# Kernel tuning notes

Measured on AMD Instinct MI355X. Metric: run time of the kernel, lower is better.

Reference implementation:

```python
import jax, jax.numpy as jnp
import numpy as np

HID = 128          # hidden_dim
NEV = 16           # n_eigenvectors
CURV = 1.0         # curvature
MAX_NORM = 0.95
N_SCALES = 3


def setup_inputs() -> dict:
    key = jax.random.key(0)
    ks = jax.random.split(key, 12)
    B, N, D = 2048, 128, 64
    A = jax.random.uniform(ks[0], (B, N, N), dtype=jnp.float32)
    A = 0.5 * (A + jnp.swapaxes(A, -1, -2))  # symmetric nonnegative adjacency
    nf = jax.random.normal(ks[1], (B, N, D), dtype=jnp.float32)
    s = 0.05
    return {
        'adjacency': A,
        'node_features': nf,
        'scale_weights': jnp.ones((N_SCALES,), jnp.float32) / N_SCALES,
        'curvature_scale': jnp.array(1.0, jnp.float32),
        'sp_w1': jax.random.normal(ks[2], (NEV, HID), jnp.float32) * s,
        'sp_b1': jnp.zeros((HID,), jnp.float32),
        'sp_w2': jax.random.normal(ks[3], (HID, HID // 2), jnp.float32) * s,
        'sp_b2': jnp.zeros((HID // 2,), jnp.float32),
        'out_w1': jax.random.normal(ks[4], (HID, HID), jnp.float32) * s,
        'out_b1': jnp.zeros((HID,), jnp.float32),
        'out_w2': jax.random.normal(ks[5], (HID, 16), jnp.float32) * s,
        'out_b2': jnp.zeros((16,), jnp.float32),
    }


def reference(adjacency, node_features, scale_weights, curvature_scale,
              sp_w1, sp_b1, sp_w2, sp_b2, out_w1, out_b1, out_w2, out_b2):
    B, N, _ = adjacency.shape
    deg = adjacency.sum(axis=-1)                         # (B, N)
    # normalized Laplacian  L = I - D^{-1/2} A D^{-1/2}
    d_is = (deg + 1e-8) ** -0.5
    sym_adj = adjacency * d_is[:, :, None] * d_is[:, None, :]
    L = jnp.eye(N, dtype=adjacency.dtype) - sym_adj
    evals, evecs = jnp.linalg.eigh(L)                    # ascending, like torch
    k = min(NEV, N - 1)
    sel_vals = evals[:, 1:k + 1]                         # (B, k)  skip trivial eig
    sel_vecs = evecs[:, :, 1:k + 1]                      # (B, N, k)
    # spectral pooling: softmax over -eigenvalues, weighted sum of eigenvectors over nodes
    w = jax.nn.softmax(-sel_vals, axis=-1)               # (B, k)
    pooled = (sel_vecs * w[:, None, :]).sum(axis=1)      # (B, k)
    spectral = jnp.maximum(pooled @ sp_w1 + sp_b1, 0.0) @ sp_w2 + sp_b2  # (B, HID//2)
    # multi-scale diffusion with row-normalized adjacency
    row_adj = adjacency / (deg + 1e-8)[:, :, None]
    ws = jax.nn.softmax(scale_weights)
    feats = node_features
    ms = ws[0] * feats.mean(axis=1)                      # (B, D) with D == HID//2
    for s in range(1, N_SCALES):
        feats = jnp.einsum('bij,bjd->bid', row_adj, feats)
        ms = ms + ws[s] * feats.mean(axis=1)
    combined = jnp.concatenate([spectral, ms], axis=-1)  # (B, HID)
    z_euclidean = jnp.maximum(combined @ out_w1 + out_b1, 0.0) @ out_w2 + out_b2
    # Poincare ball projection (curvature value used as detached scalar, like .item())
    c = CURV * jax.nn.sigmoid(curvature_scale)
    c_const = jax.lax.stop_gradient(c)
    norm = jnp.linalg.norm(z_euclidean, axis=-1, keepdims=True)
    max_r = MAX_NORM / jnp.sqrt(c_const)
    z = z_euclidean * jnp.minimum(1.0, max_r / (norm + 1e-12))
    return z, z_euclidean, spectral, sel_vals, c
```

## Files before the change

### kernel.cpp

```cpp
#include <hip/hip_runtime.h>
#include <math.h>

#define NN 128
#define BLK 256

__device__ __forceinline__ float hsum4(float4 v) { return (v.x + v.y) + (v.z + v.w); }

__device__ __forceinline__ float bcast(float v, int lane) {
  return __int_as_float(__builtin_amdgcn_readlane(__float_as_int(v), lane));
}

__device__ __forceinline__ float waveRedF(float v) {
#pragma unroll
  for (int off = 32; off > 0; off >>= 1) v += __shfl_down(v, off, 64);
  return v;
}
__device__ __forceinline__ float waveAllRedF(float v) {
#pragma unroll
  for (int off = 32; off > 0; off >>= 1) v += __shfl_xor(v, off, 64);
  return v;
}
__device__ __forceinline__ float getc(float4 a, int c) {
  return (c == 0) ? a.x : (c == 1) ? a.y : (c == 2) ? a.z : a.w;
}
__device__ __forceinline__ float blockReduceSumF(float v, float* redf, int tid) {
  v = waveRedF(v);
  __syncthreads();
  if ((tid & 63) == 0) redf[tid >> 6] = v;
  __syncthreads();
  return (redf[0] + redf[1]) + (redf[2] + redf[3]);
}
__device__ __forceinline__ float startvec(int i, int k) {
  unsigned h = (unsigned)(i * 1664525 + k * 1013904223 + 12345);
  h ^= h >> 13; h *= 2654435761u; h ^= h >> 16;
  return ((float)(h & 0xFFFFFFu) * (1.0f / 16777216.0f)) - 0.5f;
}

extern "C" __global__ void __launch_bounds__(BLK, 4)
holo_kernel(const float* __restrict__ A, const float* __restrict__ F,
            const float* __restrict__ swg, const float* __restrict__ curv,
            const float* __restrict__ W1, const float* __restrict__ Bb1,
            const float* __restrict__ W2, const float* __restrict__ Bb2,
            const float* __restrict__ OW1, const float* __restrict__ OB1,
            const float* __restrict__ OW2, const float* __restrict__ OB2,
            float* __restrict__ out, int B)
{
  __shared__ __align__(16) float wsA[NN * 17];
  __shared__ __align__(16) float wsB[NN * 17];
  __shared__ unsigned swb[16 * 5];
  __shared__ float  ddf[NN], eef[NN];
  __shared__ float  tvecf[NN];
  __shared__ float  redf[4];
  __shared__ double sc[8];
  __shared__ float  redupf[2], redutf[2], redsigf[2];
  __shared__ float  lamf[20], blof[17], bhif[17];
  __shared__ float  ssvf[16], dredf[16];
  __shared__ float  msv[64], pool[16], zrow[16];

  double* dscr  = (double*)wsA;
  float* svec   = wsA + 512;
  float* invdeg = wsA + 640;
  float* gvv    = wsA + 768;
  float* cw     = wsA + 896;
  float* ubuf   = wsA + 1024;
  float* pbuf   = wsA + 1152;
  float* colk   = wsA + 1280;
  float* byv    = wsA;
  float* fscr   = wsB;
  float* cornr  = wsB + 256;
  float* sA     = wsB;
  float* comb   = wsB;
  float* hbuf   = wsB + 128;
  unsigned char* bcnt = (unsigned char*)swb;

  const int  tid  = threadIdx.x;
  const int  r    = tid & 127;
  const int  h    = tid >> 7;
  const int  lane = tid & 63;
  const int  widm = tid >> 6;
  const long b    = blockIdx.x;
  const float* Ab = A + b * (long)(NN * NN);
  const float* Fb = F + b * (long)(NN * 64);

  float4 areg[16];
  {
    const float4* Arow = reinterpret_cast<const float4*>(Ab + (long)r * NN) + 16 * h;
#pragma unroll
    for (int uu = 0; uu < 16; ++uu) areg[uu] = Arow[uu];
  }
  if (tid == 0) {
    const float a0 = swg[0], a1 = swg[1], a2 = swg[2];
    const float mx = fmaxf(a0, fmaxf(a1, a2));
    const float e0 = expf(a0 - mx), e1 = expf(a1 - mx), e2v = expf(a2 - mx);
    const float s = e0 + e1 + e2v;
    sc[0] = (double)(e0 / s); sc[1] = (double)(e1 / s); sc[2] = (double)(e2v / s);
  }
  {
    float4 s4 = make_float4(0.f, 0.f, 0.f, 0.f);
#pragma unroll
    for (int uu = 0; uu < 16; ++uu) {
      s4.x += areg[uu].x; s4.y += areg[uu].y; s4.z += areg[uu].z; s4.w += areg[uu].w;
    }
    dscr[tid] = (double)hsum4(s4);
  }
  __syncthreads();
  if (tid < NN) {
    const double dg = dscr[tid] + dscr[tid + NN] + 1e-8;
    invdeg[tid] = (float)(1.0 / dg);
    svec[tid]   = (float)(1.0 / sqrt(dg));
  }
  __syncthreads();
  {
    const float4* iv4 = (const float4*)invdeg;
    float4 acc = make_float4(0.f, 0.f, 0.f, 0.f);
#pragma unroll
    for (int uu = 0; uu < 16; ++uu) {
      const float4 a = areg[uu], w = iv4[16 * h + uu];
      acc.x = fmaf(a.x, w.x, acc.x); acc.y = fmaf(a.y, w.y, acc.y);
      acc.z = fmaf(a.z, w.z, acc.z); acc.w = fmaf(a.w, w.w, acc.w);
    }
    fscr[tid] = hsum4(acc);
  }
  __syncthreads();
  if (tid < NN) {
    const float gv = fscr[tid] + fscr[tid + NN];
    gvv[tid] = gv;
    ubuf[tid] = gv * invdeg[tid];
  }
  __syncthreads();
  {
    const float4* ub4 = (const float4*)ubuf;
    float4 acc = make_float4(0.f, 0.f, 0.f, 0.f);
#pragma unroll
    for (int uu = 0; uu < 16; ++uu) {
      const float4 a = areg[uu], w = ub4[16 * h + uu];
      acc.x = fmaf(a.x, w.x, acc.x); acc.y = fmaf(a.y, w.y, acc.y);
      acc.z = fmaf(a.z, w.z, acc.z); acc.w = fmaf(a.w, w.w, acc.w);
    }
    fscr[tid] = hsum4(acc);
  }
  __syncthreads();
  if (tid < NN) {
    const float hv = fscr[tid] + fscr[tid + NN];
    cw[tid] = ((float)sc[0] + (float)sc[1] * gvv[tid] + (float)sc[2] * hv) * (1.0f / NN);
  }
  __syncthreads();
  {
    const int d = tid & 63, qt = tid >> 6;
    float acc = 0.0f;
    const float* fb = Fb + qt * 32 * 64;
    for (int n = 0; n < 32; ++n) acc = fmaf(cw[qt * 32 + n], fb[n * 64 + d], acc);
    fscr[tid] = acc;
  }
  __syncthreads();
  if (tid < 64) msv[tid] = (fscr[tid] + fscr[64 + tid]) + (fscr[128 + tid] + fscr[192 + tid]);

  {
    const float sr = svec[r];
    const float4* sv4p = (const float4*)svec;
#pragma unroll
    for (int uu = 0; uu < 16; ++uu) {
      const float4 sv = sv4p[16 * h + uu];
      float4 a = areg[uu];
      a.x = -a.x * sr * sv.x; a.y = -a.y * sr * sv.y;
      a.z = -a.z * sr * sv.z; a.w = -a.w * sr * sv.w;
      areg[uu] = a;
    }
    if ((r >> 6) == h) {
      const int cl = r & 63, du = cl >> 2, dc = cl & 3;
#pragma unroll
      for (int uu = 0; uu < 16; ++uu) if (uu == du) {
        float4 a = areg[uu];
        a.x += (dc == 0) ? 1.f : 0.f; a.y += (dc == 1) ? 1.f : 0.f;
        a.z += (dc == 2) ? 1.f : 0.f; a.w += (dc == 3) ? 1.f : 0.f;
        areg[uu] = a;
      }
    }
  }
  if (tid < NN) tvecf[tid] = 1.0f;
  if (h == 0) {
    const float v0 = areg[0].x;
    colk[r] = v0;
    if (r == 0) ddf[0] = v0;
    const float s = waveRedF((r >= 2) ? v0 * v0 : 0.f);
    if (lane == 0) redsigf[widm] = s;
  }
  __syncthreads();

  for (int k = 0; k < 95; ++k) {
    const float sigma  = redsigf[0] + redsigf[1];
    const float alphaf = colk[k + 1];
    float betaf, tauf, sclf;
    if (sigma <= 0.f) { betaf = alphaf; tauf = 0.f; sclf = 0.f; }
    else {
      betaf = (float)(-copysign(sqrt((double)alphaf * (double)alphaf + (double)sigma),
                                (double)alphaf));
      tauf = (betaf - alphaf) / betaf;
      sclf = 1.0f / (alphaf - betaf);
    }
    if (tid == 0) eef[k] = betaf;
    if (h == 0) ubuf[r] = (r <= k) ? 0.f : (r == k + 1) ? 1.f : colk[r] * sclf;
    __syncthreads();
    {
      float4 acc = make_float4(0.f, 0.f, 0.f, 0.f);
      if (r >= k + 1 && 64 * h + 63 >= k + 1 && tauf != 0.f) {
        const float4* ub4 = (const float4*)ubuf;
#pragma unroll
        for (int uu = 0; uu < 16; ++uu) {
          if (64 * h + 4 * uu + 3 >= k + 1) {
            const float4 a = areg[uu], u4 = ub4[16 * h + uu];
            acc.x = fmaf(a.x, u4.x, acc.x); acc.y = fmaf(a.y, u4.y, acc.y);
            acc.z = fmaf(a.z, u4.z, acc.z); acc.w = fmaf(a.w, u4.w, acc.w);
          }
        }
      }
      fscr[tid] = hsum4(acc);
    }
    __syncthreads();
    if (h == 0) {
      const float p = tauf * (fscr[r] + fscr[r + NN]);
      pbuf[r] = p;
      const float uv = ubuf[r];
      const float s1 = waveRedF(uv * p);
      const float s2 = waveRedF(uv * tvecf[r]);
      if (lane == 0) { redupf[widm] = s1; redutf[widm] = s2; }
    }
    __syncthreads();
    {
      const float K   = 0.5f * tauf * (redupf[0] + redupf[1]);
      const float tut = tauf * (redutf[0] + redutf[1]);
      if (r >= k + 1) {
        const float ur = ubuf[r];
        const float qr = fmaf(-K, ur, pbuf[r]);
        if (64 * h + 63 >= k + 1) {
          const float4* ub4 = (const float4*)ubuf;
          const float4* pb4 = (const float4*)pbuf;
#pragma unroll
          for (int uu = 0; uu < 16; ++uu) {
            if (64 * h + 4 * uu + 3 >= k + 1) {
              const float4 u4 = ub4[16 * h + uu], p4 = pb4[16 * h + uu];
              float4 a = areg[uu];
              const float qx = fmaf(-K, u4.x, p4.x);
              const float qy = fmaf(-K, u4.y, p4.y);
              const float qz = fmaf(-K, u4.z, p4.z);
              const float qw = fmaf(-K, u4.w, p4.w);
              a.x -= ur * qx + qr * u4.x;
              a.y -= ur * qy + qr * u4.y;
              a.z -= ur * qz + qr * u4.z;
              a.w -= ur * qw + qr * u4.w;
              areg[uu] = a;
            }
          }
        }
        if (h == 0) tvecf[r] -= tut * ubuf[r];
      }
      const int hstar = (k + 1) >> 6;
      if (h == hstar) {
        float sigp = 0.0f;
        if (r >= k + 1) {
          const int cl = (k + 1) - 64 * hstar, du = cl >> 2, dc = cl & 3;
          float val = 0.f;
#pragma unroll
          for (int uu = 0; uu < 16; ++uu) if (uu == du) val = getc(areg[uu], dc);
          if (r == k + 1) ddf[k + 1] = val;
          else {
            colk[r] = val;
            if (r >= k + 3) sigp = val * val;
          }
        }
        const float s = waveRedF(sigp);
        if (lane == 0) redsigf[widm & 1] = s;
      }
    }
    __syncthreads();
  }

  if (h == 1 && r >= 96) {
    const int rl = r - 96;
#pragma unroll
    for (int uu = 8; uu < 16; ++uu) {
      const int j0 = (uu - 8) * 4;
      cornr[rl * 33 + j0 + 0] = areg[uu].x;
      cornr[rl * 33 + j0 + 1] = areg[uu].y;
      cornr[rl * 33 + j0 + 2] = areg[uu].z;
      cornr[rl * 33 + j0 + 3] = areg[uu].w;
    }
  }
  __syncthreads();

  if (tid < 64) {
    const bool own = (lane < 32);
    float arow[32];
#pragma unroll
    for (int j = 0; j < 32; ++j) arow[j] = own ? cornr[lane * 33 + j] : 0.f;
    float colval = own ? colk[96 + lane] : 0.f;
    float tv     = own ? tvecf[96 + lane] : 0.f;

    for (int k = 95; k <= 125; ++k) {
      const int kk = k - 95;
      const float sigp  = (lane >= kk + 1 && lane < 32) ? colval * colval : 0.f;
      const float sigma = waveAllRedF(sigp);
      const float alphaf = bcast(colval, kk);
      float betaf, tauf, sclf;
      if (sigma <= 0.f) { betaf = alphaf; tauf = 0.f; sclf = 0.f; }
      else {
        betaf = -copysignf(sqrtf(fmaf(alphaf, alphaf, sigma)), alphaf);
        tauf = (betaf - alphaf) / betaf;
        sclf = 1.0f / (alphaf - betaf);
      }
      if (lane == 0) eef[k] = betaf;
      const bool live = own && (lane >= kk);
      const float u_me = !live ? 0.f : (lane == kk ? 1.f : colval * sclf);
      float y = 0.f;
#pragma unroll
      for (int j = 0; j < 32; ++j) y = fmaf(arow[j], bcast(u_me, j), y);
      const float p_me = live ? tauf * y : 0.f;
      const float up = waveAllRedF(u_me * p_me);
      const float ut = waveAllRedF(u_me * tv);
      const float K   = 0.5f * tauf * up;
      const float tut = tauf * ut;
      const float q_me = fmaf(-K, u_me, p_me);
      tv -= tut * u_me;
      float ncol = 0.f;
#pragma unroll
      for (int j = 0; j < 32; ++j) {
        const float uj = bcast(u_me, j);
        const float qj = bcast(q_me, j);
        arow[j] -= u_me * qj + q_me * uj;
        if (j == kk) ncol = arow[j];
      }
      if (lane == 0) ddf[k + 1] = bcast(ncol, kk);
      colval = (lane > kk && lane < 32) ? ncol : 0.f;
    }
    const float e126 = bcast(colval, 31);
    const float d127 = bcast(arow[31], 31);
    if (lane == 0) { eef[NN - 2] = e126; ddf[NN - 1] = d127; }
    if (own) tvecf[96 + lane] = tv;
  }
  __syncthreads();

  if (tid == 0) {
    double lo = 1e30, hi = -1e30;
    for (int i = 0; i < NN; ++i) {
      const double rr = ((i > 0) ? fabs((double)eef[i - 1]) : 0.0)
                      + ((i < NN - 1) ? fabs((double)eef[i]) : 0.0);
      lo = fmin(lo, (double)ddf[i] - rr);
      hi = fmax(hi, (double)ddf[i] + rr);
    }
    sc[4] = lo - 1e-6; sc[5] = hi + 1e-6;
  }
  __syncthreads();
  if (tid < 17) { blof[tid] = (float)sc[4]; bhif[tid] = (float)sc[5]; }
  __syncthreads();
  for (int round = 0; round < 11; ++round) {
    if (tid < 119) {
      const int ke = tid / 7, j = tid % 7;
      const double lo = (double)blof[ke], hi = (double)bhif[ke];
      const double x = lo + (hi - lo) * ((double)(j + 1) * 0.125);
      int cnt = 0;
      double pm = 1.0, p = (double)ddf[0] - x;
      if (p < 0.0) cnt++;
      for (int i = 1; i < NN; ++i) {
        const double e = (double)eef[i - 1];
        const double pn = ((double)ddf[i] - x) * p - (e * e) * pm;
        pm = p; p = pn;
        if ((p < 0.0) != (pm < 0.0)) cnt++;
        const double ap = fabs(p);
        if (ap > 1e100)                   { p *= 1e-100; pm *= 1e-100; }
        else if (ap < 1e-100 && ap > 0.0) { p *= 1e100;  pm *= 1e100; }
      }
      bcnt[tid] = (unsigned char)cnt;
    }
    __syncthreads();
    if (tid < 17) {
      const float lo = blof[tid], hi = bhif[tid];
      const float w8 = (hi - lo) * 0.125f;
      float nlo = lo, nhi = hi;
      for (int jj = 0; jj < 7; ++jj) {
        const float x = lo + w8 * (float)(jj + 1);
        if ((int)bcnt[tid * 7 + jj] <= tid) nlo = x; else { nhi = x; break; }
      }
      blof[tid] = nlo; bhif[tid] = nhi;
    }
    __syncthreads();
  }
  if (tid < 17) lamf[tid] = 0.5f * (blof[tid] + bhif[tid]);
  __syncthreads();

  if (tid < 16) {
    const double lk = (double)lamf[tid + 1];
    for (int it = 0; it < 2; ++it) {
      float beta = (float)((double)ddf[0] - lk);
      float gam  = eef[0];
      float rr   = (it == 0) ? startvec(0, tid) : byv[0 * 17 + tid];
      unsigned bw = 0;
      for (int i = 1; i < NN; ++i) {
        const int j = i - 1;
        const float ai = eef[i - 1];
        const float bi = (float)((double)ddf[i] - lk);
        const float ci = (i < NN - 1) ? eef[i] : 0.0f;
        const float ri = (it == 0) ? startvec(i, tid) : byv[i * 17 + tid];
        if (fabsf(beta) >= fabsf(ai)) {
          float piv = (beta == 0.0f) ? 1e-25f : beta;
          const float mm = ai / piv;
          sA [j * 17 + tid] = piv;
          byv[j * 17 + tid] = rr;
          beta = bi - mm * gam;  gam = ci;  rr = ri - mm * rr;
        } else {
          const float mm = beta / ai;
          sA [j * 17 + tid] = mm;
          byv[j * 17 + tid] = ri;
          beta = gam - mm * bi;  gam = -mm * ci;  rr = rr - mm * ri;
          bw |= 1u << (j & 31);
        }
        if ((j & 31) == 31) { swb[tid * 5 + (j >> 5)] = bw; bw = 0; }
      }
      if (beta == 0.0f) beta = 1e-25f;
      sA [127 * 17 + tid] = beta;
      byv[127 * 17 + tid] = rr;
      swb[tid * 5 + 3] = bw;
      float y1 = 0.0f, y2 = 0.0f;
      for (int j = NN - 1; j >= 0; --j) {
        const bool sj = (swb[tid * 5 + (j >> 5)] >> (j & 31)) & 1;
        const bool sjm1 = (j > 0) ? ((swb[tid * 5 + ((j - 1) >> 5)] >> ((j - 1) & 31)) & 1) : false;
        float u0, u1, u2;
        if (sj) {
          u0 = eef[j];
          u1 = (float)((double)ddf[j + 1] - lk);
          u2 = (j < NN - 2) ? eef[j + 1] : 0.0f;
        } else {
          u0 = sA[j * 17 + tid];
          const float ej = (j < NN - 1) ? eef[j] : 0.0f;
          u1 = sjm1 ? (-sA[(j - 1) * 17 + tid] * ej) : ej;
          u2 = 0.0f;
        }
        const float yy = (byv[j * 17 + tid] - u1 * y1 - u2 * y2) / u0;
        byv[j * 17 + tid] = yy;
        y2 = y1; y1 = yy;
      }
      double nrm = 0.0;
      for (int i = 0; i < NN; ++i) { const double v = (double)byv[i * 17 + tid]; nrm += v * v; }
      const double inv = 1.0 / sqrt(nrm);
      for (int i = 0; i < NN; ++i) byv[i * 17 + tid] = (float)((double)byv[i * 17 + tid] * inv);
    }
  }
  __syncthreads();

  for (int kk = 1; kk < 16; ++kk) {
    const int j = tid >> 3, s8 = tid & 7;
    float part = 0.0f;
    if (j < kk)
      for (int i = s8 * 16; i < s8 * 16 + 16; ++i)
        part += byv[i * 17 + j] * byv[i * 17 + kk];
    for (int off = 4; off > 0; off >>= 1) part += __shfl_down(part, off, 8);
    __syncthreads();
    if (s8 == 0 && j < kk) dredf[j] = part;
    __syncthreads();
    if (tid < NN) {
      float acc = byv[tid * 17 + kk];
      for (int j2 = 0; j2 < kk; ++j2) acc -= dredf[j2] * byv[tid * 17 + j2];
      byv[tid * 17 + kk] = acc;
    }
    __syncthreads();
    float p2 = 0.0f;
    if (tid < NN) { const float v = byv[tid * 17 + kk]; p2 = v * v; }
    const float n2 = blockReduceSumF(p2, redf, tid);
    if (tid < NN) byv[tid * 17 + kk] = byv[tid * 17 + kk] / sqrtf(n2);
    __syncthreads();
  }

  if (tid < NN) {
    const int j = tid >> 3, s8 = tid & 7;
    float part = 0.0f;
    for (int i = s8 * 16; i < s8 * 16 + 16; ++i)
      part += tvecf[i] * byv[i * 17 + j];
    for (int off = 4; off > 0; off >>= 1) part += __shfl_down(part, off, 8);
    if (s8 == 0) ssvf[j] = part;
  }
  __syncthreads();
  if (tid == 0) {
    float lv[16], ev[16];
    float mx = -1e30f;
    for (int i = 0; i < 16; ++i) { lv[i] = lamf[i + 1]; mx = fmaxf(mx, -lv[i]); }
    float se = 0.0f;
    for (int i = 0; i < 16; ++i) { ev[i] = expf(-lv[i] - mx); se += ev[i]; }
    for (int i = 0; i < 16; ++i) pool[i] = (ev[i] / se) * ssvf[i];
  }
  __syncthreads();

  if (tid < NN) {
    float acc = Bb1[tid];
    for (int i = 0; i < 16; ++i) acc = fmaf(pool[i], W1[i * 128 + tid], acc);
    hbuf[tid] = fmaxf(acc, 0.0f);
  }
  __syncthreads();
  if (tid < 64) {
    float acc = Bb2[tid];
    for (int i = 0; i < 128; ++i) acc = fmaf(hbuf[i], W2[i * 64 + tid], acc);
    comb[tid] = acc;
  } else if (tid < NN) {
    comb[tid] = msv[tid - 64];
  }
  __syncthreads();
  if (tid < NN) {
    float acc = OB1[tid];
    for (int i = 0; i < 128; ++i) acc = fmaf(comb[i], OW1[i * 128 + tid], acc);
    hbuf[tid] = fmaxf(acc, 0.0f);
  }
  __syncthreads();
  if (tid < 16) {
    float acc = OB2[tid];
    for (int i = 0; i < 128; ++i) acc = fmaf(hbuf[i], OW2[i * 16 + tid], acc);
    zrow[tid] = acc;
  }
  __syncthreads();

  const long zeoff = (long)B * 16;
  const long spoff = (long)B * 32;
  const long svoff = (long)B * 32 + (long)B * 64;
  const long coff  = svoff + (long)B * 16;

  if (tid == 0) {
    const float c = 1.0f / (1.0f + expf(-curv[0]));
    float nrm = 0.0f;
    for (int i = 0; i < 16; ++i) nrm += zrow[i] * zrow[i];
    nrm = sqrtf(nrm);
    const float max_r = 0.95f / sqrtf(c);
    sc[3] = (double)fminf(1.0f, max_r / (nrm + 1e-12f));
    if (b == 0) out[coff] = c;
  }
  __syncthreads();
  if (tid < 16) {
    const float fac = (float)sc[3];
    out[b * 16 + tid]          = zrow[tid] * fac;
    out[zeoff + b * 16 + tid]  = zrow[tid];
    out[svoff + b * 16 + tid]  = lamf[tid + 1];
  }
  if (tid < 64) out[spoff + b * 64 + tid] = comb[tid];
}

extern "C" void kernel_launch(void* const* d_in, const int* in_sizes, int n_in,
                              void* d_out, int out_size, void* d_ws, size_t ws_size,
                              hipStream_t stream) {
  const float* A    = (const float*)d_in[0];
  const float* F    = (const float*)d_in[1];
  const float* swg  = (const float*)d_in[2];
  const float* curv = (const float*)d_in[3];
  const float* W1   = (const float*)d_in[4];
  const float* Bb1  = (const float*)d_in[5];
  const float* W2   = (const float*)d_in[6];
  const float* Bb2  = (const float*)d_in[7];
  const float* OW1  = (const float*)d_in[8];
  const float* OB1  = (const float*)d_in[9];
  const float* OW2  = (const float*)d_in[10];
  const float* OB2  = (const float*)d_in[11];
  float* out = (float*)d_out;
  const int B = in_sizes[0] / (128 * 128);

  holo_kernel<<<dim3(B), dim3(BLK), 0, stream>>>(
      A, F, swg, curv, W1, Bb1, W2, Bb2, OW1, OB1, OW2, OB2, out, B);
}
```

Measured before the change: 1.405 ms.

## Shift tridiagonalization wave-handoff earlier and fuse Gram-Schmidt norm into projection

The block-wide Householder loop now stops at column 87 instead of 95, so the single-wave register-resident tail handles a 40x40 corner instead of 32x32. This cuts the number of iterations that each need block-wide barriers, but each tail iteration does more register work. Separately, the Gram-Schmidt step computes the squared norm of the new vector from the projection coefficients (||v||^2 - sum c^2). That removes the separate block reduction and two barriers per vector. The cancellation-based norm can lose precision when vectors are nearly dependent.

```diff
diff --git a/kernel.cpp b/kernel.cpp
--- a/kernel.cpp
+++ b/kernel.cpp
@@ -3,6 +3,7 @@
 
 #define NN 128
 #define BLK 256
+#define CB  88
 
 __device__ __forceinline__ float hsum4(float4 v) { return (v.x + v.y) + (v.z + v.w); }
 
@@ -22,13 +23,6 @@
 }
 __device__ __forceinline__ float getc(float4 a, int c) {
   return (c == 0) ? a.x : (c == 1) ? a.y : (c == 2) ? a.z : a.w;
-}
-__device__ __forceinline__ float blockReduceSumF(float v, float* redf, int tid) {
-  v = waveRedF(v);
-  __syncthreads();
-  if ((tid & 63) == 0) redf[tid >> 6] = v;
-  __syncthreads();
-  return (redf[0] + redf[1]) + (redf[2] + redf[3]);
 }
 __device__ __forceinline__ float startvec(int i, int k) {
   unsigned h = (unsigned)(i * 1664525 + k * 1013904223 + 12345);
@@ -50,11 +44,10 @@
   __shared__ unsigned swb[16 * 5];
   __shared__ float  ddf[NN], eef[NN];
   __shared__ float  tvecf[NN];
-  __shared__ float  redf[4];
   __shared__ double sc[8];
   __shared__ float  redupf[2], redutf[2], redsigf[2];
   __shared__ float  lamf[20], blof[17], bhif[17];
-  __shared__ float  ssvf[16], dredf[16];
+  __shared__ float  ssvf[16], dredf[17];
   __shared__ float  msv[64], pool[16], zrow[16];
 
   double* dscr  = (double*)wsA;
@@ -187,7 +180,7 @@
   }
   __syncthreads();
 
-  for (int k = 0; k < 95; ++k) {
+  for (int k = 0; k < CB - 1; ++k) {
     const float sigma  = redsigf[0] + redsigf[1];
     const float alphaf = colk[k + 1];
     float betaf, tauf, sclf;
@@ -275,30 +268,30 @@
     __syncthreads();
   }
 
-  if (h == 1 && r >= 96) {
-    const int rl = r - 96;
-#pragma unroll
-    for (int uu = 8; uu < 16; ++uu) {
-      const int j0 = (uu - 8) * 4;
-      cornr[rl * 33 + j0 + 0] = areg[uu].x;
-      cornr[rl * 33 + j0 + 1] = areg[uu].y;
-      cornr[rl * 33 + j0 + 2] = areg[uu].z;
-      cornr[rl * 33 + j0 + 3] = areg[uu].w;
+  if (h == 1 && r >= CB) {
+    const int rl = r - CB;
+#pragma unroll
+    for (int uu = 6; uu < 16; ++uu) {
+      const int j0 = (uu - 6) * 4;
+      cornr[rl * 41 + j0 + 0] = areg[uu].x;
+      cornr[rl * 41 + j0 + 1] = areg[uu].y;
+      cornr[rl * 41 + j0 + 2] = areg[uu].z;
+      cornr[rl * 41 + j0 + 3] = areg[uu].w;
     }
   }
   __syncthreads();
 
   if (tid < 64) {
-    const bool own = (lane < 32);
-    float arow[32];
-#pragma unroll
-    for (int j = 0; j < 32; ++j) arow[j] = own ? cornr[lane * 33 + j] : 0.f;
-    float colval = own ? colk[96 + lane] : 0.f;
-    float tv     = own ? tvecf[96 + lane] : 0.f;
-
-    for (int k = 95; k <= 125; ++k) {
-      const int kk = k - 95;
-      const float sigp  = (lane >= kk + 1 && lane < 32) ? colval * colval : 0.f;
+    const bool own = (lane < 40);
+    float arow[40];
+#pragma unroll
+    for (int j = 0; j < 40; ++j) arow[j] = own ? cornr[lane * 41 + j] : 0.f;
+    float colval = own ? colk[CB + lane] : 0.f;
+    float tv     = own ? tvecf[CB + lane] : 0.f;
+
+    for (int k = CB - 1; k <= 125; ++k) {
+      const int kk = k - (CB - 1);
+      const float sigp  = (lane >= kk + 1 && lane < 40) ? colval * colval : 0.f;
       const float sigma = waveAllRedF(sigp);
       const float alphaf = bcast(colval, kk);
       float betaf, tauf, sclf;
@@ -313,7 +306,7 @@
       const float u_me = !live ? 0.f : (lane == kk ? 1.f : colval * sclf);
       float y = 0.f;
 #pragma unroll
-      for (int j = 0; j < 32; ++j) y = fmaf(arow[j], bcast(u_me, j), y);
+      for (int j = 0; j < 40; ++j) y = fmaf(arow[j], bcast(u_me, j), y);
       const float p_me = live ? tauf * y : 0.f;
       const float up = waveAllRedF(u_me * p_me);
       const float ut = waveAllRedF(u_me * tv);
@@ -323,19 +316,19 @@
       tv -= tut * u_me;
       float ncol = 0.f;
 #pragma unroll
-      for (int j = 0; j < 32; ++j) {
+      for (int j = 0; j < 40; ++j) {
         const float uj = bcast(u_me, j);
         const float qj = bcast(q_me, j);
         arow[j] -= u_me * qj + q_me * uj;
         if (j == kk) ncol = arow[j];
       }
       if (lane == 0) ddf[k + 1] = bcast(ncol, kk);
-      colval = (lane > kk && lane < 32) ? ncol : 0.f;
-    }
-    const float e126 = bcast(colval, 31);
-    const float d127 = bcast(arow[31], 31);
+      colval = (lane > kk && lane < 40) ? ncol : 0.f;
+    }
+    const float e126 = bcast(colval, 39);
+    const float d127 = bcast(arow[39], 39);
     if (lane == 0) { eef[NN - 2] = e126; ddf[NN - 1] = d127; }
-    if (own) tvecf[96 + lane] = tv;
+    if (own) tvecf[CB + lane] = tv;
   }
   __syncthreads();
 
@@ -449,23 +442,23 @@
   for (int kk = 1; kk < 16; ++kk) {
     const int j = tid >> 3, s8 = tid & 7;
     float part = 0.0f;
-    if (j < kk)
+    if (tid < NN && j <= kk)
       for (int i = s8 * 16; i < s8 * 16 + 16; ++i)
         part += byv[i * 17 + j] * byv[i * 17 + kk];
     for (int off = 4; off > 0; off >>= 1) part += __shfl_down(part, off, 8);
-    __syncthreads();
-    if (s8 == 0 && j < kk) dredf[j] = part;
+    if (tid < NN && s8 == 0 && j <= kk) dredf[j] = part;
     __syncthreads();
     if (tid < NN) {
       float acc = byv[tid * 17 + kk];
-      for (int j2 = 0; j2 < kk; ++j2) acc -= dredf[j2] * byv[tid * 17 + j2];
-      byv[tid * 17 + kk] = acc;
-    }
-    __syncthreads();
-    float p2 = 0.0f;
-    if (tid < NN) { const float v = byv[tid * 17 + kk]; p2 = v * v; }
-    const float n2 = blockReduceSumF(p2, redf, tid);
-    if (tid < NN) byv[tid * 17 + kk] = byv[tid * 17 + kk] / sqrtf(n2);
+      float n2  = dredf[kk];
+      for (int j2 = 0; j2 < kk; ++j2) {
+        const float c = dredf[j2];
+        acc -= c * byv[tid * 17 + j2];
+        n2  -= c * c;
+      }
+      n2 = fmaxf(n2, 1e-12f);
+      byv[tid * 17 + kk] = acc / sqrtf(n2);
+    }
     __syncthreads();
   }
 
```

After: 1.396 ms. No clear change (-0.6%).
